# Kernel tuning notes

Measured on AMD Instinct MI355X. Metric: run time of the kernel, lower is better.

Reference implementation:

```python
import jax, jax.numpy as jnp
import numpy as np

N, K, D, E, H = 65536, 8, 256, 256, 132  # points, components, latent_dim, encoder_dim, FC hidden

def setup_inputs() -> dict:
    key = jax.random.key(0)
    ks = jax.random.split(key, 12)
    s = 0.05
    f32 = jnp.float32
    return {
        "signal": jax.random.normal(ks[0], (N, E), f32),
        "components": jax.random.normal(ks[1], (K, N, D), f32),
        # message_map / update_map: Linear(D, D)
        "Wm": jax.random.normal(ks[2], (D, D), f32) * s,
        "bm": jnp.zeros((D,), f32),
        "Wu": jax.random.normal(ks[3], (D, D), f32) * s,
        "bu": jnp.zeros((D,), f32),
        "W0": jax.random.normal(ks[4], (H, E + D), f32) * s,
        "b0": jnp.zeros((H,), f32),
        "W1": jax.random.normal(ks[5], (H, H), f32) * s,
        "b1": jnp.zeros((H,), f32),
        "W2": jax.random.normal(ks[6], (H, H), f32) * s,
        "b2": jnpes if False else jnp.zeros((H,), f32),
        "W3": jax.random.normal(ks[7], (D, H), f32) * s,
        "b3": jnp.zeros((D,), f32),
    }

def reference(signal, components, Wm, bm, Wu, bu, W0, b0, W1, b1, W2, b2, W3, b3):
    k = components.shape[0]
    # sum_k Linear(comp_k) == Linear applied to sum, with bias counted k times (linearity)
    right = components.sum(0) @ Wm.T + k * bm          # [N, D]
    right = right @ Wu.T + bu                          # update_map
    x = jnp.concatenate([signal, right], axis=-1)      # [N, E+D]
    x = jax.nn.relu(x @ W0.T + b0)
    x = jax.nn.relu(x @ W1.T + b1)
    x = jax.nn.relu(x @ W2.T + b2)
    return x @ W3.T + b3                               # [N, D]
```

## Files before the change

kernel.cpp:

```cpp
#include <hip/hip_runtime.h>
#include <hip/hip_bf16.h>


typedef float  f32x4  __attribute__((ext_vector_type(4)));
typedef __bf16 bf16x8 __attribute__((ext_vector_type(8)));
typedef unsigned int   u32x2 __attribute__((ext_vector_type(2)));
typedef unsigned short u16x8 __attribute__((ext_vector_type(8)));

__device__ __forceinline__ unsigned short f2bf(float f) {
  unsigned int u = __builtin_bit_cast(unsigned int, f);
  u += 0x7fffu + ((u >> 16) & 1u);
  return (unsigned short)(u >> 16);
}

__device__ __forceinline__ u32x2 pack4(f32x4 v) {
  u32x2 r;
  r[0] = (unsigned)f2bf(v[0]) | ((unsigned)f2bf(v[1]) << 16);
  r[1] = (unsigned)f2bf(v[2]) | ((unsigned)f2bf(v[3]) << 16);
  return r;
}

__device__ __forceinline__ void gl16(const void* g, void* l) {
  __builtin_amdgcn_global_load_lds(
      (const __attribute__((address_space(1))) unsigned*)(unsigned long long)g,
      (__attribute__((address_space(3))) unsigned*)(unsigned)(unsigned long long)l,
      16, 0, 0);
}
__device__ __forceinline__ void gl4(const void* g, void* l) {
  __builtin_amdgcn_global_load_lds(
      (const __attribute__((address_space(1))) unsigned*)(unsigned long long)g,
      (__attribute__((address_space(3))) unsigned*)(unsigned)(unsigned long long)l,
      4, 0, 0);
}

__device__ __forceinline__ void stage10k(const char* src, char* dst,
                                         int wave, int lane) {
  const char* g0 = src + wave * 1024 + lane * 16;
  char* l0 = dst + wave * 1024;
  gl16(g0, l0);
  gl16(g0 + 4096, l0 + 4096);
  const char* g1 = src + 8192 + wave * 256 + lane * 4;
  char* l1 = dst + 8192 + wave * 256;
  gl4(g1, l1);
  gl4(g1 + 1024, l1 + 1024);
}
__device__ __forceinline__ void stage6k(const char* src, char* dst,
                                        int wave, int lane) {
  gl16(src + wave * 1024 + lane * 16, dst + wave * 1024);
  const char* g1 = src + 4096 + wave * 256 + lane * 4;
  char* l1 = dst + 4096 + wave * 256;
  gl4(g1, l1);
  gl4(g1 + 1024, l1 + 1024);
}

__global__ __launch_bounds__(256) void kP(
    const float* __restrict__ W0, const float* __restrict__ Wu,
    const float* __restrict__ Wm, const float* __restrict__ bm,
    const float* __restrict__ bu, const float* __restrict__ b0,
    const float* __restrict__ b1, const float* __restrict__ b2,
    float* __restrict__ Wc, float* __restrict__ bias1,
    float* __restrict__ b1p, float* __restrict__ b2p) {
  const int b = blockIdx.x;
  const int d = threadIdx.x;
  if (b < 132) {
    __shared__ float u[256];
    const int h = b;
    float s = 0.f;
#pragma unroll 8
    for (int i = 0; i < 256; ++i) s += W0[h * 512 + 256 + i] * Wu[i * 256 + d];
    u[d] = s;
    __syncthreads();
    float s2 = 0.f;
#pragma unroll 8
    for (int j = 0; j < 256; ++j) s2 += u[j] * Wm[j * 256 + d];
    Wc[h * 256 + d] = s2;
  } else {
    __shared__ float bml[256];
    __shared__ float rbl[256];
    bml[d] = bm[d];
    __syncthreads();
    {
      const f32x4* wr = (const f32x4*)(Wu + d * 256);
      const f32x4* bm4 = (const f32x4*)bml;
      float s = 0.f;
#pragma unroll 8
      for (int i = 0; i < 64; ++i) {
        f32x4 w = wr[i], v = bm4[i];
        s += w[0] * v[0] + w[1] * v[1] + w[2] * v[2] + w[3] * v[3];
      }
      rbl[d] = 8.f * s + bu[d];
    }
    __syncthreads();
    if (d < 160) {
      float v = 0.f;
      if (d < 132) {
        float s = 0.f;
#pragma unroll 8
        for (int j = 0; j < 256; ++j) s += W0[d * 512 + 256 + j] * rbl[j];
        v = b0[d] + s;
      }
      bias1[d] = v;
      b1p[d] = (d < 132) ? b1[d] : 0.f;
      b2p[d] = (d < 132) ? b2[d] : 0.f;
    }
  }
}

__global__ __launch_bounds__(256) void kC(
    const float* __restrict__ W0, const float* __restrict__ Wc,
    const float* __restrict__ W1, const float* __restrict__ W2,
    const float* __restrict__ W3,
    unsigned short* __restrict__ P1, unsigned short* __restrict__ P2,
    unsigned short* __restrict__ P3, unsigned short* __restrict__ P4) {
  int e = blockIdx.x * 256 + threadIdx.x;
  if (e >= 174080) return;
  unsigned short* dst; int NT, rel, mode;
  if (e < 81920)       { dst = P1; NT = 10; rel = e;          mode = 0; }
  else if (e < 107520) { dst = P2; NT = 10; rel = e - 81920;  mode = 1; }
  else if (e < 133120) { dst = P3; NT = 10; rel = e - 107520; mode = 2; }
  else                 { dst = P4; NT = 16; rel = e - 133120; mode = 3; }
  int chunk = rel >> 9, q = rel & 511;
  int lane = q >> 3, j = q & 7;
  int kk = chunk / NT, nt = chunk - kk * NT;
  int k = kk * 32 + (lane >> 4) * 8 + j;
  int n = nt * 16 + (lane & 15);
  float v = 0.f;
  if (mode == 0) {
    if (n < 132) v = (k < 256) ? W0[n * 512 + k] : Wc[n * 256 + (k - 256)];
  } else if (mode == 1) {
    if (n < 132 && k < 132) v = W1[n * 132 + k];
  } else if (mode == 2) {
    if (n < 132 && k < 132) v = W2[n * 132 + k];
  } else {
    if (k < 132) v = W3[n * 132 + k];
  }
  dst[rel] = f2bf(v);
}

__global__ __launch_bounds__(256, 3) void kD(
    const float* __restrict__ signal, const float* __restrict__ comp,
    const unsigned short* __restrict__ Pseq,
    const float* __restrict__ bias1, const float* __restrict__ b1p,
    const float* __restrict__ b2p, const float* __restrict__ b3,
    float* __restrict__ out) {
  extern __shared__ char lds[];
  const int tid = threadIdx.x;
  const int wave = tid >> 6;
  const int lane = tid & 63;
  const int lhalf = lane >> 4;
  const int l16 = lane & 15;
  char* act = lds + wave * 8192;
  char* wbA = lds + 32768;
  char* wbB = lds + 32768 + 10240;
  const char* Pb = (const char*)Pseq;
  const int row0 = ((int)blockIdx.x * 4 + wave) * 16;
  const int asw = (l16 & 7) << 4;

  {
    f32x4 sg[16];
    const f32x4* sp = (const f32x4*)signal;
#pragma unroll
    for (int r = 0; r < 16; ++r) sg[r] = sp[(size_t)(row0 + r) * 64 + lane];
#pragma unroll
    for (int r = 0; r < 16; ++r)
      *(u32x2*)(act + r * 512 + ((lane * 8) ^ ((r & 7) << 4))) = pack4(sg[r]);
  }

  stage10k(Pb, wbA, wave, lane);
  __syncthreads();

  const int r2 = lane >> 5, c32 = lane & 31;
  const f32x4* cp = (const f32x4*)comp;
  u16x8 cs[8];

  f32x4 acc[10];
#pragma unroll
  for (int i = 0; i < 10; ++i) acc[i] = f32x4{0.f, 0.f, 0.f, 0.f};

#pragma unroll
  for (int kk = 0; kk < 8; ++kk) {
    stage10k(Pb + (kk + 1) * 10240, (((kk + 1) & 1) ? wbB : wbA), wave, lane);
    f32x4 t[16];
    {
      const size_t rbase = (size_t)(row0 + 2 * kk + r2) * 64 + c32 * 2;
#pragma unroll
      for (int k = 0; k < 8; ++k) {
        t[2 * k]     = cp[(size_t)k * 4194304u + rbase];
        t[2 * k + 1] = cp[(size_t)k * 4194304u + rbase + 1];
      }
    }
    char* wb = (kk & 1) ? wbB : wbA;
    bf16x8 af = *(const bf16x8*)(act + l16 * 512 + ((kk * 64 + lhalf * 16) ^ asw));
#pragma unroll
    for (int nt = 0; nt < 10; ++nt)
      acc[nt] = __builtin_amdgcn_mfma_f32_16x16x32_bf16(
          af, *(const bf16x8*)(wb + nt * 1024 + lane * 16), acc[nt], 0, 0, 0);
    {
      f32x4 s0 = (t[0] + t[2]) + (t[4] + t[6]);
      s0 = s0 + ((t[8] + t[10]) + (t[12] + t[14]));
      f32x4 s1 = (t[1] + t[3]) + (t[5] + t[7]);
      s1 = s1 + ((t[9] + t[11]) + (t[13] + t[15]));
      u16x8 v;
      v[0] = f2bf(s0[0]); v[1] = f2bf(s0[1]);
      v[2] = f2bf(s0[2]); v[3] = f2bf(s0[3]);
      v[4] = f2bf(s1[0]); v[5] = f2bf(s1[1]);
      v[6] = f2bf(s1[2]); v[7] = f2bf(s1[3]);
      cs[kk] = v;
    }
    __syncthreads();
  }

  asm volatile("" ::: "memory");
#pragma unroll
  for (int j = 0; j < 8; ++j) {
    const int rw = 2 * j + r2;
    *(u16x8*)(act + rw * 512 + ((c32 * 16) ^ ((rw & 7) << 4))) = cs[j];
  }
  asm volatile("" ::: "memory");

#pragma unroll
  for (int kk = 8; kk < 16; ++kk) {
    if (kk < 15)
      stage10k(Pb + (kk + 1) * 10240, (((kk + 1) & 1) ? wbB : wbA), wave, lane);
    else
      stage10k(Pb + 163840, wbA, wave, lane);
    char* wb = (kk & 1) ? wbB : wbA;
    bf16x8 af =
        *(const bf16x8*)(act + l16 * 512 + (((kk - 8) * 64 + lhalf * 16) ^ asw));
#pragma unroll
    for (int nt = 0; nt < 10; ++nt)
      acc[nt] = __builtin_amdgcn_mfma_f32_16x16x32_bf16(
          af, *(const bf16x8*)(wb + nt * 1024 + lane * 16), acc[nt], 0, 0, 0);
    __syncthreads();
  }

  {
    float bv[10];
#pragma unroll
    for (int nt = 0; nt < 10; ++nt) bv[nt] = bias1[nt * 16 + l16];
    asm volatile("" ::: "memory");
#pragma unroll
    for (int nt = 0; nt < 10; ++nt) {
#pragma unroll
      for (int r = 0; r < 4; ++r) {
        const int row = lhalf * 4 + r;
        float v = fmaxf(acc[nt][r] + bv[nt], 0.f);
        *(unsigned short*)(act + row * 512 +
                           (((nt * 16 + l16) * 2) ^ ((row & 7) << 4))) = f2bf(v);
      }
    }
    asm volatile("" ::: "memory");
  }

#pragma unroll
  for (int L = 0; L < 2; ++L) {
    const char* hb = Pb + (L ? 215040 : 163840);
    const float* hbias = L ? b2p : b1p;
#pragma unroll
    for (int i = 0; i < 10; ++i) acc[i] = f32x4{0.f, 0.f, 0.f, 0.f};
#pragma unroll
    for (int kk = 0; kk < 5; ++kk) {
      const char* nsrc = (kk < 4) ? (hb + (kk + 1) * 10240)
                                  : (L ? (Pb + 266240) : (Pb + 215040));
      stage10k(nsrc, (((kk + L + 1) & 1) ? wbB : wbA), wave, lane);
      char* wb = ((kk + L) & 1) ? wbB : wbA;
      bf16x8 af =
          *(const bf16x8*)(act + l16 * 512 + ((kk * 64 + lhalf * 16) ^ asw));
#pragma unroll
      for (int nt = 0; nt < 10; ++nt)
        acc[nt] = __builtin_amdgcn_mfma_f32_16x16x32_bf16(
            af, *(const bf16x8*)(wb + nt * 1024 + lane * 16), acc[nt], 0, 0, 0);
      __syncthreads();
    }
    float bv[10];
#pragma unroll
    for (int nt = 0; nt < 10; ++nt) bv[nt] = hbias[nt * 16 + l16];
    asm volatile("" ::: "memory");
#pragma unroll
    for (int nt = 0; nt < 10; ++nt) {
#pragma unroll
      for (int r = 0; r < 4; ++r) {
        const int row = lhalf * 4 + r;
        float v = fmaxf(acc[nt][r] + bv[nt], 0.f);
        *(unsigned short*)(act + row * 512 +
                           (((nt * 16 + l16) * 2) ^ ((row & 7) << 4))) = f2bf(v);
      }
    }
    asm volatile("" ::: "memory");
  }

  f32x4 a4[16];
#pragma unroll
  for (int i = 0; i < 16; ++i) a4[i] = f32x4{0.f, 0.f, 0.f, 0.f};
  const char* P4b = Pb + 266240;
#pragma unroll
  for (int kk = 0; kk < 5; ++kk) {
    stage6k(P4b + kk * 16384 + 10240, wbB, wave, lane);
    bf16x8 af =
        *(const bf16x8*)(act + l16 * 512 + ((kk * 64 + lhalf * 16) ^ asw));
#pragma unroll
    for (int nt = 0; nt < 10; ++nt)
      a4[nt] = __builtin_amdgcn_mfma_f32_16x16x32_bf16(
          af, *(const bf16x8*)(wbA + nt * 1024 + lane * 16), a4[nt], 0, 0, 0);
    __syncthreads();
    if (kk < 4) stage10k(P4b + (kk + 1) * 16384, wbA, wave, lane);
#pragma unroll
    for (int nt = 10; nt < 16; ++nt)
      a4[nt] = __builtin_amdgcn_mfma_f32_16x16x32_bf16(
          af, *(const bf16x8*)(wbB + (nt - 10) * 1024 + lane * 16), a4[nt], 0, 0, 0);
    __syncthreads();
  }

  float bv[16];
#pragma unroll
  for (int nt = 0; nt < 16; ++nt) bv[nt] = b3[nt * 16 + l16];
  float* op = out + (size_t)(row0 + lhalf * 4) * 256 + l16;
#pragma unroll
  for (int nt = 0; nt < 16; ++nt) {
#pragma unroll
    for (int r = 0; r < 4; ++r)
      op[(size_t)r * 256 + nt * 16] = a4[nt][r] + bv[nt];
  }
}

extern "C" void kernel_launch(void* const* d_in, const int* in_sizes, int n_in,
                              void* d_out, int out_size, void* d_ws, size_t ws_size,
                              hipStream_t stream) {
  const float* signal = (const float*)d_in[0];
  const float* comp   = (const float*)d_in[1];
  const float* Wm = (const float*)d_in[2];
  const float* bm = (const float*)d_in[3];
  const float* Wu = (const float*)d_in[4];
  const float* bu = (const float*)d_in[5];
  const float* W0 = (const float*)d_in[6];
  const float* b0 = (const float*)d_in[7];
  const float* W1 = (const float*)d_in[8];
  const float* b1 = (const float*)d_in[9];
  const float* W2 = (const float*)d_in[10];
  const float* b2 = (const float*)d_in[11];
  const float* W3 = (const float*)d_in[12];
  const float* b3 = (const float*)d_in[13];

  char* ws = (char*)d_ws;
  float* Wc    = (float*)(ws + 0);
  float* bias1 = (float*)(ws + 135168);
  float* b1p   = (float*)(ws + 135808);
  float* b2p   = (float*)(ws + 136448);
  unsigned short* P1 = (unsigned short*)(ws + 137216);
  unsigned short* P2 = (unsigned short*)(ws + 301056);
  unsigned short* P3 = (unsigned short*)(ws + 352256);
  unsigned short* P4 = (unsigned short*)(ws + 403456);

  hipLaunchKernelGGL(kP, dim3(133), dim3(256), 0, stream,
                     W0, Wu, Wm, bm, bu, b0, b1, b2, Wc, bias1, b1p, b2p);
  hipLaunchKernelGGL(kC, dim3(680), dim3(256), 0, stream,
                     W0, Wc, W1, W2, W3, P1, P2, P3, P4);
  hipLaunchKernelGGL(kD, dim3(1024), dim3(256), 53248, stream,
                     signal, comp, P1, bias1, b1p, b2p, b3, (float*)d_out);
}
```

Baseline: 199.5 us.

## Load MFMA weight fragments straight to registers, drop LDS staging and barriers

Each wave now reads its weight B-fragments directly from global memory into double-buffered VGPR arrays, where before they were staged through shared LDS buffers with block-wide __syncthreads. The component-sum loads are rebuilt as a rolling 4-deep software prefetch ring so they overlap the MFMA work. The intent is to remove barrier stalls and LDS traffic, and to cut the LDS allocation from 53248 to 32768 bytes. In exchange every wave re-reads the weights from L2, register pressure rises sharply, and launch bounds drop from 3 to 2 blocks per SM, which may lower occupancy.

```diff
diff --git a/kernel.cpp b/kernel.cpp
--- a/kernel.cpp
+++ b/kernel.cpp
@@ -18,39 +18,6 @@
   r[0] = (unsigned)f2bf(v[0]) | ((unsigned)f2bf(v[1]) << 16);
   r[1] = (unsigned)f2bf(v[2]) | ((unsigned)f2bf(v[3]) << 16);
   return r;
-}
-
-__device__ __forceinline__ void gl16(const void* g, void* l) {
-  __builtin_amdgcn_global_load_lds(
-      (const __attribute__((address_space(1))) unsigned*)(unsigned long long)g,
-      (__attribute__((address_space(3))) unsigned*)(unsigned)(unsigned long long)l,
-      16, 0, 0);
-}
-__device__ __forceinline__ void gl4(const void* g, void* l) {
-  __builtin_amdgcn_global_load_lds(
-      (const __attribute__((address_space(1))) unsigned*)(unsigned long long)g,
-      (__attribute__((address_space(3))) unsigned*)(unsigned)(unsigned long long)l,
-      4, 0, 0);
-}
-
-__device__ __forceinline__ void stage10k(const char* src, char* dst,
-                                         int wave, int lane) {
-  const char* g0 = src + wave * 1024 + lane * 16;
-  char* l0 = dst + wave * 1024;
-  gl16(g0, l0);
-  gl16(g0 + 4096, l0 + 4096);
-  const char* g1 = src + 8192 + wave * 256 + lane * 4;
-  char* l1 = dst + 8192 + wave * 256;
-  gl4(g1, l1);
-  gl4(g1 + 1024, l1 + 1024);
-}
-__device__ __forceinline__ void stage6k(const char* src, char* dst,
-                                        int wave, int lane) {
-  gl16(src + wave * 1024 + lane * 16, dst + wave * 1024);
-  const char* g1 = src + 4096 + wave * 256 + lane * 4;
-  char* l1 = dst + 4096 + wave * 256;
-  gl4(g1, l1);
-  gl4(g1 + 1024, l1 + 1024);
 }
 
 __global__ __launch_bounds__(256) void kP(
@@ -137,7 +104,26 @@
   dst[rel] = f2bf(v);
 }
 
-__global__ __launch_bounds__(256, 3) void kD(
+#define WISS(BUF, CHUNK)                                                     \
+  {                                                                          \
+    _Pragma("unroll") for (int nt = 0; nt < 10; ++nt)                        \
+        BUF[nt] = *(const bf16x8*)(Pb + (CHUNK) * 10240 + nt * 1024 +        \
+                                   lane * 16);                               \
+  }
+#define WISS8(BUF, HALF)                                                     \
+  {                                                                          \
+    _Pragma("unroll") for (int nt = 0; nt < 8; ++nt)                         \
+        BUF[nt] = *(const bf16x8*)(Pb + 266240 + (HALF) * 8192 + nt * 1024 + \
+                                   lane * 16);                               \
+  }
+#define MFMA10(BUF)                                                          \
+  {                                                                          \
+    _Pragma("unroll") for (int nt = 0; nt < 10; ++nt)                        \
+        acc[nt] = __builtin_amdgcn_mfma_f32_16x16x32_bf16(af, BUF[nt],       \
+                                                          acc[nt], 0, 0, 0); \
+  }
+
+__global__ __launch_bounds__(256, 2) void kD(
     const float* __restrict__ signal, const float* __restrict__ comp,
     const unsigned short* __restrict__ Pseq,
     const float* __restrict__ bias1, const float* __restrict__ b1p,
@@ -150,64 +136,64 @@
   const int lhalf = lane >> 4;
   const int l16 = lane & 15;
   char* act = lds + wave * 8192;
-  char* wbA = lds + 32768;
-  char* wbB = lds + 32768 + 10240;
   const char* Pb = (const char*)Pseq;
   const int row0 = ((int)blockIdx.x * 4 + wave) * 16;
   const int asw = (l16 & 7) << 4;
-
-  {
-    f32x4 sg[16];
-    const f32x4* sp = (const f32x4*)signal;
-#pragma unroll
-    for (int r = 0; r < 16; ++r) sg[r] = sp[(size_t)(row0 + r) * 64 + lane];
-#pragma unroll
-    for (int r = 0; r < 16; ++r)
-      *(u32x2*)(act + r * 512 + ((lane * 8) ^ ((r & 7) << 4))) = pack4(sg[r]);
-  }
-
-  stage10k(Pb, wbA, wave, lane);
-  __syncthreads();
-
   const int r2 = lane >> 5, c32 = lane & 31;
   const f32x4* cp = (const f32x4*)comp;
+  const size_t cbase = (size_t)(row0 + r2) * 64 + c32 * 2;
+
+  f32x4 sg[16];
+  const f32x4* sp = (const f32x4*)signal;
+#pragma unroll
+  for (int r = 0; r < 16; ++r) sg[r] = sp[(size_t)(row0 + r) * 64 + lane];
+
+  bf16x8 wA[10], wB[10];
+  WISS(wA, 0);
+
+  f32x4 ct[4][2];
+#pragma unroll
+  for (int s = 0; s < 4; ++s) {
+    ct[s][0] = cp[cbase + (size_t)s * 4194304u];
+    ct[s][1] = cp[cbase + (size_t)s * 4194304u + 1];
+  }
+
+#pragma unroll
+  for (int r = 0; r < 16; ++r)
+    *(u32x2*)(act + r * 512 + ((lane * 8) ^ ((r & 7) << 4))) = pack4(sg[r]);
+
+  f32x4 acc[10];
+#pragma unroll
+  for (int i = 0; i < 10; ++i) acc[i] = f32x4{0.f, 0.f, 0.f, 0.f};
+  f32x4 ca0, ca1;
   u16x8 cs[8];
 
-  f32x4 acc[10];
-#pragma unroll
-  for (int i = 0; i < 10; ++i) acc[i] = f32x4{0.f, 0.f, 0.f, 0.f};
-
 #pragma unroll
   for (int kk = 0; kk < 8; ++kk) {
-    stage10k(Pb + (kk + 1) * 10240, (((kk + 1) & 1) ? wbB : wbA), wave, lane);
-    f32x4 t[16];
+    if (kk & 1) { WISS(wA, kk + 1); } else { WISS(wB, kk + 1); }
+#pragma unroll
+    for (int i = 0; i < 8; ++i) {
+      const int s = kk * 8 + i;
+      const int b4 = s & 3;
+      if (i == 0) { ca0 = ct[b4][0]; ca1 = ct[b4][1]; }
+      else        { ca0 += ct[b4][0]; ca1 += ct[b4][1]; }
+      if (s + 4 < 64) {
+        const int j2 = (s + 4) >> 3, k2 = (s + 4) & 7;
+        ct[b4][0] = cp[cbase + (size_t)k2 * 4194304u + j2 * 128];
+        ct[b4][1] = cp[cbase + (size_t)k2 * 4194304u + j2 * 128 + 1];
+      }
+    }
     {
-      const size_t rbase = (size_t)(row0 + 2 * kk + r2) * 64 + c32 * 2;
-#pragma unroll
-      for (int k = 0; k < 8; ++k) {
-        t[2 * k]     = cp[(size_t)k * 4194304u + rbase];
-        t[2 * k + 1] = cp[(size_t)k * 4194304u + rbase + 1];
-      }
-    }
-    char* wb = (kk & 1) ? wbB : wbA;
-    bf16x8 af = *(const bf16x8*)(act + l16 * 512 + ((kk * 64 + lhalf * 16) ^ asw));
-#pragma unroll
-    for (int nt = 0; nt < 10; ++nt)
-      acc[nt] = __builtin_amdgcn_mfma_f32_16x16x32_bf16(
-          af, *(const bf16x8*)(wb + nt * 1024 + lane * 16), acc[nt], 0, 0, 0);
-    {
-      f32x4 s0 = (t[0] + t[2]) + (t[4] + t[6]);
-      s0 = s0 + ((t[8] + t[10]) + (t[12] + t[14]));
-      f32x4 s1 = (t[1] + t[3]) + (t[5] + t[7]);
-      s1 = s1 + ((t[9] + t[11]) + (t[13] + t[15]));
       u16x8 v;
-      v[0] = f2bf(s0[0]); v[1] = f2bf(s0[1]);
-      v[2] = f2bf(s0[2]); v[3] = f2bf(s0[3]);
-      v[4] = f2bf(s1[0]); v[5] = f2bf(s1[1]);
-      v[6] = f2bf(s1[2]); v[7] = f2bf(s1[3]);
+      v[0] = f2bf(ca0[0]); v[1] = f2bf(ca0[1]);
+      v[2] = f2bf(ca0[2]); v[3] = f2bf(ca0[3]);
+      v[4] = f2bf(ca1[0]); v[5] = f2bf(ca1[1]);
+      v[6] = f2bf(ca1[2]); v[7] = f2bf(ca1[3]);
       cs[kk] = v;
     }
-    __syncthreads();
+    bf16x8 af =
+        *(const bf16x8*)(act + l16 * 512 + ((kk * 64 + lhalf * 16) ^ asw));
+    if (kk & 1) { MFMA10(wB); } else { MFMA10(wA); }
   }
 
   asm volatile("" ::: "memory");
@@ -220,18 +206,10 @@
 
 #pragma unroll
   for (int kk = 8; kk < 16; ++kk) {
-    if (kk < 15)
-      stage10k(Pb + (kk + 1) * 10240, (((kk + 1) & 1) ? wbB : wbA), wave, lane);
-    else
-      stage10k(Pb + 163840, wbA, wave, lane);
-    char* wb = (kk & 1) ? wbB : wbA;
-    bf16x8 af =
-        *(const bf16x8*)(act + l16 * 512 + (((kk - 8) * 64 + lhalf * 16) ^ asw));
-#pragma unroll
-    for (int nt = 0; nt < 10; ++nt)
-      acc[nt] = __builtin_amdgcn_mfma_f32_16x16x32_bf16(
-          af, *(const bf16x8*)(wb + nt * 1024 + lane * 16), acc[nt], 0, 0, 0);
-    __syncthreads();
+    if (kk & 1) { WISS(wA, kk + 1); } else { WISS(wB, kk + 1); }
+    bf16x8 af = *(const bf16x8*)(act + l16 * 512 +
+                                 (((kk - 8) * 64 + lhalf * 16) ^ asw));
+    if (kk & 1) { MFMA10(wB); } else { MFMA10(wA); }
   }
 
   {
@@ -252,25 +230,23 @@
     asm volatile("" ::: "memory");
   }
 
+  bf16x8 w4A[8], w4B[8];
 #pragma unroll
   for (int L = 0; L < 2; ++L) {
-    const char* hb = Pb + (L ? 215040 : 163840);
     const float* hbias = L ? b2p : b1p;
 #pragma unroll
     for (int i = 0; i < 10; ++i) acc[i] = f32x4{0.f, 0.f, 0.f, 0.f};
 #pragma unroll
-    for (int kk = 0; kk < 5; ++kk) {
-      const char* nsrc = (kk < 4) ? (hb + (kk + 1) * 10240)
-                                  : (L ? (Pb + 266240) : (Pb + 215040));
-      stage10k(nsrc, (((kk + L + 1) & 1) ? wbB : wbA), wave, lane);
-      char* wb = ((kk + L) & 1) ? wbB : wbA;
+    for (int q = 0; q < 5; ++q) {
+      const int c = 16 + L * 5 + q;
+      if (c < 25) {
+        if (c & 1) { WISS(wA, c + 1); } else { WISS(wB, c + 1); }
+      } else {
+        WISS8(w4A, 0);
+      }
       bf16x8 af =
-          *(const bf16x8*)(act + l16 * 512 + ((kk * 64 + lhalf * 16) ^ asw));
-#pragma unroll
-      for (int nt = 0; nt < 10; ++nt)
-        acc[nt] = __builtin_amdgcn_mfma_f32_16x16x32_bf16(
-            af, *(const bf16x8*)(wb + nt * 1024 + lane * 16), acc[nt], 0, 0, 0);
-      __syncthreads();
+          *(const bf16x8*)(act + l16 * 512 + ((q * 64 + lhalf * 16) ^ asw));
+      if (c & 1) { MFMA10(wB); } else { MFMA10(wA); }
     }
     float bv[10];
 #pragma unroll
@@ -292,23 +268,23 @@
   f32x4 a4[16];
 #pragma unroll
   for (int i = 0; i < 16; ++i) a4[i] = f32x4{0.f, 0.f, 0.f, 0.f};
-  const char* P4b = Pb + 266240;
-#pragma unroll
-  for (int kk = 0; kk < 5; ++kk) {
-    stage6k(P4b + kk * 16384 + 10240, wbB, wave, lane);
-    bf16x8 af =
-        *(const bf16x8*)(act + l16 * 512 + ((kk * 64 + lhalf * 16) ^ asw));
-#pragma unroll
-    for (int nt = 0; nt < 10; ++nt)
-      a4[nt] = __builtin_amdgcn_mfma_f32_16x16x32_bf16(
-          af, *(const bf16x8*)(wbA + nt * 1024 + lane * 16), a4[nt], 0, 0, 0);
-    __syncthreads();
-    if (kk < 4) stage10k(P4b + (kk + 1) * 16384, wbA, wave, lane);
-#pragma unroll
-    for (int nt = 10; nt < 16; ++nt)
-      a4[nt] = __builtin_amdgcn_mfma_f32_16x16x32_bf16(
-          af, *(const bf16x8*)(wbB + (nt - 10) * 1024 + lane * 16), a4[nt], 0, 0, 0);
-    __syncthreads();
+#pragma unroll
+  for (int h = 0; h < 10; ++h) {
+    if (h < 9) {
+      if (h & 1) { WISS8(w4A, h + 1); } else { WISS8(w4B, h + 1); }
+    }
+    bf16x8 af = *(const bf16x8*)(act + l16 * 512 +
+                                 (((h >> 1) * 64 + lhalf * 16) ^ asw));
+#pragma unroll
+    for (int i = 0; i < 8; ++i) {
+      const int nt = (h & 1) * 8 + i;
+      if (h & 1)
+        a4[nt] = __builtin_amdgcn_mfma_f32_16x16x32_bf16(af, w4B[i], a4[nt],
+                                                         0, 0, 0);
+      else
+        a4[nt] = __builtin_amdgcn_mfma_f32_16x16x32_bf16(af, w4A[i], a4[nt],
+                                                         0, 0, 0);
+    }
   }
 
   float bv[16];
@@ -355,6 +331,6 @@
                      W0, Wu, Wm, bm, bu, b0, b1, b2, Wc, bias1, b1p, b2p);
   hipLaunchKernelGGL(kC, dim3(680), dim3(256), 0, stream,
                      W0, Wc, W1, W2, W3, P1, P2, P3, P4);
-  hipLaunchKernelGGL(kD, dim3(1024), dim3(256), 53248, stream,
+  hipLaunchKernelGGL(kD, dim3(1024), dim3(256), 32768, stream,
                      signal, comp, P1, bias1, b1p, b2p, b3, (float*)d_out);
 }
```

New measurement: 201.4 us. No clear change (+0.9%).
